# Kernel tuning notes

Hardware: AMD Instinct MI355X
Metric: run time of the kernel (lower is better)

The kernel has to match this reference:

```python
import jax, jax.numpy as jnp
import numpy as np

NUM_HEADS = 16   # matches init_kwargs
WARP_Q = 32      # per-warp Q quant granularity (rows)
BLK_K = 64       # per-block K quant granularity (rows)
EPS = 1e-8


def setup_inputs() -> dict:
    key = jax.random.key(0)
    kq, kk, kv = jax.random.split(key, 3)
    b, s, hid = 2, 2048, 2048
    q = jax.random.normal(kq, (b, s, hid), jnp.float32)
    k = jax.random.normal(kk, (b, s, hid), jnp.float32)
    v = jax.random.normal(kv, (b, s, hid), jnp.float32)
    return {"q": q, "k": k, "v": v, "window_left": 1024, "window_right": 1024}


def _quant_int8(x, group):
    # x: [b, h, s, d] -> int8-valued floats + per-row scales [b, h, s, 1]
    b, h, s, d = x.shape
    xg = x.reshape(b, h, s // group, group, d)
    scale = jnp.maximum(jnp.max(jnp.abs(xg), axis=(3, 4), keepdims=True) / 127.0, EPS)
    xq = jnp.clip(jnp.round(xg / scale), -127.0, 127.0)
    scale_rows = jnp.broadcast_to(scale, (b, h, s // group, group, 1)).reshape(b, h, s, 1)
    return xq.reshape(b, h, s, d), scale_rows


def _sage_attention(q, k, v, window_left, window_right):
    b, s, hid = q.shape
    n = NUM_HEADS
    d = hid // n
    sm_scale = 1.0 / np.sqrt(d)
    # [b, s, n*d] -> [b, n, s, d]
    qh = q.reshape(b, s, n, d).transpose(0, 2, 1, 3)
    kh = k.reshape(b, s, n, d).transpose(0, 2, 1, 3)
    vh = v.reshape(b, s, n, d).transpose(0, 2, 1, 3)

    # smooth K: subtract per-channel seq mean (softmax-invariant)
    k_mean = jnp.mean(kh, axis=2, keepdims=True)
    ks = kh - k_mean

    # per-warp int8 quantization of Q and K
    qq, q_scale = _quant_int8(qh, WARP_Q)
    kq, k_scale = _quant_int8(ks, BLK_K)

    # int8 QK^T, dequantized: [b, n, s, s]
    scores = jnp.einsum('bhid,bhjd->bhij', qq, kq)
    scores = scores * q_scale * jnp.swapaxes(k_scale, -1, -2) * sm_scale

    # sliding window mask (window < 0 means unlimited on that side)
    i = jnp.arange(s)[:, None]
    j = jnp.arange(s)[None, :]
    allowed = jnp.ones((s, s), dtype=bool)
    if window_left >= 0:
        allowed = allowed & ((i - j) <= window_left)
    if window_right >= 0:
        allowed = allowed & ((j - i) <= window_right)
    scores = jnp.where(allowed, scores, -jnp.inf)

    p = jax.nn.softmax(scores, axis=-1)

    # smooth V + fp16 PV accumulation
    v_mean = jnp.mean(vh, axis=2, keepdims=True)
    out16 = jnp.matmul(p.astype(jnp.float16), (vh - v_mean).astype(jnp.float16),
                       preferred_element_type=jnp.float16)
    out = out16.astype(jnp.float32) + v_mean  # rows of p sum to 1

    # [b, n, s, d] -> [b, s, n*d]
    return out.transpose(0, 2, 1, 3).reshape(b, s, n * d)


def reference(q, k, v, window_left, window_right):
    return _sage_attention(q, k, v, window_left, window_right)
```

## Files before the change

### kernel.cpp

```cpp
#include <hip/hip_runtime.h>
#include <hip/hip_fp16.h>
#include <math.h>

#define S_LEN 2048
#define NHID  2048
#define D_HEAD 128
#define N_BH  32
#define EPS_Q 1e-8f

typedef _Float16 half8 __attribute__((ext_vector_type(8)));
typedef _Float16 half4 __attribute__((ext_vector_type(4)));
typedef float floatx4 __attribute__((ext_vector_type(4)));

__global__ void means_kernel(const float* __restrict__ kk, const float* __restrict__ vv,
                             float* __restrict__ ksumP, float* __restrict__ vsumP) {
  int blk = blockIdx.x;
  int bh = blk >> 4, chunk = blk & 15;
  int b = bh >> 4, h = bh & 15;
  int t = threadIdx.x;
  int d4 = t & 31, sg = t >> 5;
  int s0 = chunk * 128;
  const long base = ((long)(b * S_LEN + s0)) * NHID + h * D_HEAD + d4 * 4;
  floatx4 ks = {0.f,0.f,0.f,0.f}, vs = {0.f,0.f,0.f,0.f};
  #pragma unroll 4
  for (int j = 0; j < 16; ++j) {
    long idx = base + (long)(sg * 16 + j) * NHID;
    ks += *(const floatx4*)(kk + idx);
    vs += *(const floatx4*)(vv + idx);
  }
  __shared__ floatx4 red[256];
  red[t] = ks; __syncthreads();
  if (t < 128) red[t] += red[t + 128]; __syncthreads();
  if (t < 64)  red[t] += red[t + 64];  __syncthreads();
  if (t < 32) *(floatx4*)(ksumP + (long)blk * 128 + t * 4) = red[t] + red[t + 32];
  __syncthreads();
  red[t] = vs; __syncthreads();
  if (t < 128) red[t] += red[t + 128]; __syncthreads();
  if (t < 64)  red[t] += red[t + 64];  __syncthreads();
  if (t < 32) *(floatx4*)(vsumP + (long)blk * 128 + t * 4) = red[t] + red[t + 32];
}

__global__ void prep_kernel(const float* __restrict__ q, const float* __restrict__ k,
                            const float* __restrict__ v,
                            const float* __restrict__ ksumP, const float* __restrict__ vsumP,
                            _Float16* __restrict__ qq, _Float16* __restrict__ kq,
                            _Float16* __restrict__ vt,
                            float* __restrict__ qscale, float* __restrict__ kscale,
                            float* __restrict__ vmean) {
  int blk = blockIdx.x;
  int t = threadIdx.x;
  int lane = t & 63, wid = t >> 6;
  __shared__ float wred[4];
  __shared__ __align__(16) _Float16 tile[64 * 136];
  int d4 = t & 31, sg = t >> 5;

  if (blk < 2048) {
    int bh = blk >> 6, g = blk & 63;
    int b = bh >> 4, h = bh & 15;
    int s0 = g * 32;
    const long gbase = ((long)(b * S_LEN + s0)) * NHID + h * D_HEAD + d4 * 4;
    floatx4 vals[4]; float am = 0.f;
    #pragma unroll
    for (int j = 0; j < 4; ++j) {
      floatx4 x = *(const floatx4*)(q + gbase + (long)(sg + j * 8) * NHID);
      vals[j] = x;
      am = fmaxf(am, fmaxf(fmaxf(fabsf(x[0]), fabsf(x[1])), fmaxf(fabsf(x[2]), fabsf(x[3]))));
    }
    #pragma unroll
    for (int off = 1; off < 64; off <<= 1) am = fmaxf(am, __shfl_xor(am, off, 64));
    if (lane == 0) wred[wid] = am;
    __syncthreads();
    am = fmaxf(fmaxf(wred[0], wred[1]), fmaxf(wred[2], wred[3]));
    float scale = fmaxf(am / 127.0f, EPS_Q);
    if (t == 0) qscale[bh * 64 + g] = scale;
    float inv = 1.0f / scale;
    #pragma unroll
    for (int j = 0; j < 4; ++j) {
      half4 hv;
      #pragma unroll
      for (int c = 0; c < 4; ++c)
        hv[c] = (_Float16)fminf(fmaxf(rintf(vals[j][c] * inv), -127.f), 127.f);
      *(half4*)(qq + ((long)bh * S_LEN + s0 + sg + j * 8) * D_HEAD + d4 * 4) = hv;
    }
  } else if (blk < 3072) {
    int bb = blk - 2048;
    int bh = bb >> 5, g = bb & 31;
    int b = bh >> 4, h = bh & 15;
    int s0 = g * 64;
    floatx4 msum = {0.f,0.f,0.f,0.f};
    #pragma unroll
    for (int c = 0; c < 16; ++c)
      msum += *(const floatx4*)(ksumP + (long)(bh * 16 + c) * 128 + d4 * 4);
    floatx4 mean = msum * (1.0f / 2048.0f);
    const long gbase = ((long)(b * S_LEN + s0)) * NHID + h * D_HEAD + d4 * 4;
    floatx4 vals[8]; float am = 0.f;
    #pragma unroll
    for (int j = 0; j < 8; ++j) {
      floatx4 x = *(const floatx4*)(k + gbase + (long)(sg + j * 8) * NHID) - mean;
      vals[j] = x;
      am = fmaxf(am, fmaxf(fmaxf(fabsf(x[0]), fabsf(x[1])), fmaxf(fabsf(x[2]), fabsf(x[3]))));
    }
    #pragma unroll
    for (int off = 1; off < 64; off <<= 1) am = fmaxf(am, __shfl_xor(am, off, 64));
    if (lane == 0) wred[wid] = am;
    __syncthreads();
    am = fmaxf(fmaxf(wred[0], wred[1]), fmaxf(wred[2], wred[3]));
    float scale = fmaxf(am / 127.0f, EPS_Q);
    if (t == 0) kscale[bh * 32 + g] = scale;
    float inv = 1.0f / scale;
    #pragma unroll
    for (int j = 0; j < 8; ++j) {
      half4 hv;
      #pragma unroll
      for (int c = 0; c < 4; ++c)
        hv[c] = (_Float16)fminf(fmaxf(rintf(vals[j][c] * inv), -127.f), 127.f);
      *(half4*)(kq + ((long)bh * S_LEN + s0 + sg + j * 8) * D_HEAD + d4 * 4) = hv;
    }
  } else {
    int bb = blk - 3072;
    int bh = bb >> 5, st = bb & 31;
    int b = bh >> 4, h = bh & 15;
    int s0 = st * 64;
    floatx4 msum = {0.f,0.f,0.f,0.f};
    #pragma unroll
    for (int c = 0; c < 16; ++c)
      msum += *(const floatx4*)(vsumP + (long)(bh * 16 + c) * 128 + d4 * 4);
    floatx4 mean = msum * (1.0f / 2048.0f);
    if (st == 0 && sg == 0)
      *(floatx4*)(vmean + bh * D_HEAD + d4 * 4) = mean;
    const long gbase = ((long)(b * S_LEN + s0)) * NHID + h * D_HEAD + d4 * 4;
    #pragma unroll
    for (int j = 0; j < 8; ++j) {
      floatx4 x = *(const floatx4*)(v + gbase + (long)(sg + j * 8) * NHID) - mean;
      half4 hv = { (_Float16)x[0], (_Float16)x[1], (_Float16)x[2], (_Float16)x[3] };
      *(half4*)(tile + (sg + j * 8) * 136 + d4 * 4) = hv;
    }
    __syncthreads();
    int dr = t >> 1, sh = (t & 1) * 32;
    _Float16* dst = vt + ((long)bh * D_HEAD + dr) * S_LEN + s0 + sh;
    #pragma unroll
    for (int jo = 0; jo < 4; ++jo) {
      union { half8 v8; _Float16 h[8]; } u;
      #pragma unroll
      for (int ji = 0; ji < 8; ++ji) u.h[ji] = tile[(sh + jo * 8 + ji) * 136 + dr];
      *(half8*)(dst + jo * 8) = u.v8;
    }
  }
}

__launch_bounds__(256, 2)
__global__ void attn_kernel(const _Float16* __restrict__ qq, const _Float16* __restrict__ kq,
                            const _Float16* __restrict__ vt,
                            const float* __restrict__ qscale, const float* __restrict__ kscale,
                            const float* __restrict__ vmean,
                            const int* __restrict__ wlp, const int* __restrict__ wrp,
                            float* __restrict__ out) {
  int bid = blockIdx.x;
  int xcd = bid & 7, rest = bid >> 3;
  int bh = xcd * 4 + (rest & 3);
  int qb = rest >> 2;
  int b = bh >> 4, h = bh & 15;
  int q0 = qb * 128;

  int wl = *wlp; if (wl < 0) wl = S_LEN;
  int wr = *wrp; if (wr < 0) wr = S_LEN;

  int t = threadIdx.x;
  int wv = t >> 6;
  int lane = t & 63;
  int ln = lane & 15;
  int qd = lane >> 4;

  int r0 = q0 + wv * 32;

  __shared__ __align__(16) _Float16 Kl[64 * 128];
  __shared__ __align__(16) _Float16 Vl[128 * 64];

  half8 qa[2][4];
  #pragma unroll
  for (int mh = 0; mh < 2; ++mh) {
    const _Float16* qbase = qq + ((long)bh * S_LEN + r0 + mh * 16 + ln) * D_HEAD + qd * 8;
    #pragma unroll
    for (int ks = 0; ks < 4; ++ks)
      qa[mh][ks] = *(const half8*)(qbase + ks * 32);
  }
  float qs = qscale[bh * 64 + (r0 >> 5)];

  float mrow[2];
  floatx4 lacc[2];
  floatx4 oacc[2][8];
  #pragma unroll
  for (int mh = 0; mh < 2; ++mh) {
    mrow[mh] = -1e30f;
    #pragma unroll
    for (int r = 0; r < 4; ++r) lacc[mh][r] = 0.f;
    #pragma unroll
    for (int nd = 0; nd < 8; ++nd) oacc[mh][nd] = (floatx4){0.f,0.f,0.f,0.f};
  }

  int lo = q0 - wl; if (lo < 0) lo = 0;
  int hi = q0 + 127 + wr; if (hi > S_LEN - 1) hi = S_LEN - 1;
  int t_lo = lo >> 6, t_hi = hi >> 6;

  const float sm_scale = 0.08838834764831845f;
  const _Float16* kbase = kq + (long)bh * S_LEN * D_HEAD;
  const _Float16* vbase = vt + (long)bh * D_HEAD * S_LEN;
  const float* kscb = kscale + bh * 32;
  const half8 vones = { (_Float16)1, (_Float16)1, (_Float16)1, (_Float16)1,
                        (_Float16)1, (_Float16)1, (_Float16)1, (_Float16)1 };

  half8 kpre[4], vpre[4];
  {
    int j0 = t_lo * 64;
    #pragma unroll
    for (int c = 0; c < 4; ++c) {
      int gc = t + c * 256;
      kpre[c] = *(const half8*)(kbase + (long)(j0 + (gc >> 4)) * D_HEAD + (gc & 15) * 8);
      vpre[c] = *(const half8*)(vbase + (long)(gc >> 3) * S_LEN + j0 + (gc & 7) * 8);
    }
  }

  for (int tt = t_lo; tt <= t_hi; ++tt) {
    int j0 = tt * 64;
    __syncthreads();
    #pragma unroll
    for (int c = 0; c < 4; ++c) {
      int gc = t + c * 256;
      {
        int row = gc >> 4, ci = gc & 15;
        int cs = (ci & 8) | ((ci ^ row) & 7);
        *(half8*)(Kl + row * 128 + cs * 8) = kpre[c];
      }
      {
        int row = gc >> 3, ci = gc & 7;
        int cs = (ci ^ row) & 7;
        *(half8*)(Vl + row * 64 + cs * 8) = vpre[c];
      }
    }
    __syncthreads();
    if (tt < t_hi) {
      int j1 = j0 + 64;
      #pragma unroll
      for (int c = 0; c < 4; ++c) {
        int gc = t + c * 256;
        kpre[c] = *(const half8*)(kbase + (long)(j1 + (gc >> 4)) * D_HEAD + (gc & 15) * 8);
        vpre[c] = *(const half8*)(vbase + (long)(gc >> 3) * S_LEN + j1 + (gc & 7) * 8);
      }
    }

    if (j0 + 63 < r0 - wl || j0 > r0 + 31 + wr) continue;

    float dscale = qs * kscb[tt] * sm_scale;

    floatx4 sacc[2][4];
    #pragma unroll
    for (int mh = 0; mh < 2; ++mh)
      #pragma unroll
      for (int nb = 0; nb < 4; ++nb) sacc[mh][nb] = (floatx4){0.f,0.f,0.f,0.f};
    #pragma unroll
    for (int nb = 0; nb < 4; ++nb)
      #pragma unroll
      for (int ks = 0; ks < 4; ++ks) {
        int ci = ks * 4 + qd;
        int cs = (ci & 8) | ((ci ^ ln) & 7);
        half8 kf = *(const half8*)(Kl + (nb * 16 + ln) * 128 + cs * 8);
        sacc[0][nb] = __builtin_amdgcn_mfma_f32_16x16x32_f16(kf, qa[0][ks], sacc[0][nb], 0, 0, 0);
        sacc[1][nb] = __builtin_amdgcn_mfma_f32_16x16x32_f16(kf, qa[1][ks], sacc[1][nb], 0, 0, 0);
      }

    half8 pa[2][2];
    #pragma unroll
    for (int mh = 0; mh < 2; ++mh) {
      int rb = r0 + mh * 16;
      bool need_mask = (j0 < rb + 15 - wl) || (j0 + 63 > rb + wr);
      int row = rb + ln;
      float sv[4][4];
      float mnb[4];
      #pragma unroll
      for (int nb = 0; nb < 4; ++nb) {
        #pragma unroll
        for (int r = 0; r < 4; ++r) {
          float s = sacc[mh][nb][r] * dscale;
          if (need_mask) {
            int col = j0 + nb * 16 + qd * 4 + r;
            bool ok = (row - col <= wl) && (col - row <= wr);
            s = ok ? s : -1e30f;
          }
          sv[nb][r] = s;
        }
        mnb[nb] = fmaxf(fmaxf(sv[nb][0], sv[nb][1]), fmaxf(sv[nb][2], sv[nb][3]));
      }
      float mx = fmaxf(fmaxf(mnb[0], mnb[1]), fmaxf(mnb[2], mnb[3]));
      mx = fmaxf(mx, __shfl_xor(mx, 16, 64));
      mx = fmaxf(mx, __shfl_xor(mx, 32, 64));

      if (__any(mx > mrow[mh] + 8.0f)) {
        float mnew = fmaxf(mrow[mh], mx);
        float alpha = __expf(mrow[mh] - mnew);
        mrow[mh] = mnew;
        float ar[4];
        #pragma unroll
        for (int r = 0; r < 4; ++r) ar[r] = __shfl(alpha, qd * 4 + r, 64);
        #pragma unroll
        for (int nd = 0; nd < 8; ++nd) {
          floatx4 o = oacc[mh][nd];
          #pragma unroll
          for (int r = 0; r < 4; ++r) o[r] *= ar[r];
          oacc[mh][nd] = o;
        }
        #pragma unroll
        for (int r = 0; r < 4; ++r) lacc[mh][r] *= ar[r];
      }

      float m0 = mrow[mh];
      #pragma unroll
      for (int ks = 0; ks < 2; ++ks) {
        half8 tf;
        #pragma unroll
        for (int r = 0; r < 4; ++r) {
          tf[r]     = (_Float16)__expf(sv[2 * ks][r] - m0);
          tf[4 + r] = (_Float16)__expf(sv[2 * ks + 1][r] - m0);
        }
        pa[mh][ks] = tf;
      }
    }

    #pragma unroll
    for (int nd = 0; nd < 8; ++nd) {
      int rowv = nd * 16 + ln;
      #pragma unroll
      for (int ks = 0; ks < 2; ++ks) {
        int ci0 = ks * 4 + (qd >> 1);
        int o4 = (qd & 1) * 4;
        int cs0 = (ci0 ^ rowv) & 7;
        int cs1 = ((ci0 + 2) ^ rowv) & 7;
        half4 v0 = *(const half4*)(Vl + rowv * 64 + cs0 * 8 + o4);
        half4 v1 = *(const half4*)(Vl + rowv * 64 + cs1 * 8 + o4);
        half8 vf = { v0[0], v0[1], v0[2], v0[3], v1[0], v1[1], v1[2], v1[3] };
        oacc[0][nd] = __builtin_amdgcn_mfma_f32_16x16x32_f16(pa[0][ks], vf, oacc[0][nd], 0, 0, 0);
        oacc[1][nd] = __builtin_amdgcn_mfma_f32_16x16x32_f16(pa[1][ks], vf, oacc[1][nd], 0, 0, 0);
      }
    }
    #pragma unroll
    for (int mh = 0; mh < 2; ++mh) {
      lacc[mh] = __builtin_amdgcn_mfma_f32_16x16x32_f16(pa[mh][0], vones, lacc[mh], 0, 0, 0);
      lacc[mh] = __builtin_amdgcn_mfma_f32_16x16x32_f16(pa[mh][1], vones, lacc[mh], 0, 0, 0);
    }
  }

  float vm[8];
  #pragma unroll
  for (int nd = 0; nd < 8; ++nd)
    vm[nd] = vmean[bh * D_HEAD + nd * 16 + ln];
  float* obase = out + ((long)b * S_LEN) * NHID + h * D_HEAD;
  #pragma unroll
  for (int mh = 0; mh < 2; ++mh)
    #pragma unroll
    for (int r = 0; r < 4; ++r) {
      int row = r0 + mh * 16 + qd * 4 + r;
      float linv = 1.0f / lacc[mh][r];
      #pragma unroll
      for (int nd = 0; nd < 8; ++nd) {
        float o16 = (float)(_Float16)(oacc[mh][nd][r] * linv);
        obase[(long)row * NHID + nd * 16 + ln] = o16 + vm[nd];
      }
    }
}

extern "C" void kernel_launch(void* const* d_in, const int* in_sizes, int n_in,
                              void* d_out, int out_size, void* d_ws, size_t ws_size,
                              hipStream_t stream) {
  (void)in_sizes; (void)n_in; (void)out_size; (void)ws_size;
  const float* q = (const float*)d_in[0];
  const float* k = (const float*)d_in[1];
  const float* v = (const float*)d_in[2];
  const int* wl = (const int*)d_in[3];
  const int* wr = (const int*)d_in[4];
  float* out = (float*)d_out;

  char* ws = (char*)d_ws;
  size_t off = 0;
  const size_t tensz = (size_t)N_BH * S_LEN * D_HEAD * sizeof(_Float16);
  _Float16* qq = (_Float16*)(ws + off); off += tensz;
  _Float16* kq = (_Float16*)(ws + off); off += tensz;
  _Float16* vt = (_Float16*)(ws + off); off += tensz;
  float* ksumP  = (float*)(ws + off); off += (size_t)N_BH * 16 * 128 * sizeof(float);
  float* vsumP  = (float*)(ws + off); off += (size_t)N_BH * 16 * 128 * sizeof(float);
  float* vmean  = (float*)(ws + off); off += N_BH * D_HEAD * sizeof(float);
  float* qscale = (float*)(ws + off); off += N_BH * 64 * sizeof(float);
  float* kscale = (float*)(ws + off); off += N_BH * 32 * sizeof(float);

  means_kernel<<<512, 256, 0, stream>>>(k, v, ksumP, vsumP);
  prep_kernel<<<4096, 256, 0, stream>>>(q, k, v, ksumP, vsumP, qq, kq, vt, qscale, kscale, vmean);
  attn_kernel<<<512, 256, 0, stream>>>(qq, kq, vt, qscale, kscale, vmean, wl, wr, out);
}
```

Measured before the change: 246.4 us.

## Split KV range across two half-blocks and merge softmax partials in shared memory

Doubles the attention block to 512 threads. Each half of the block processes half of the key tiles for the same 128 query rows, and the two partial results are merged through shared memory with a max/rescale combine (a split-K flash-decoding style). The aim is more waves in flight per CU and a shorter serial loop per block, since 512 blocks is only about two per CU. The cost is 64KB of LDS plus extra syncs and an epilogue merge, and launch_bounds(512,4) may force register spilling given the large accumulator arrays.

```diff
diff --git a/kernel.cpp b/kernel.cpp
--- a/kernel.cpp
+++ b/kernel.cpp
@@ -148,7 +148,7 @@
   }
 }
 
-__launch_bounds__(256, 2)
+__launch_bounds__(512, 4)
 __global__ void attn_kernel(const _Float16* __restrict__ qq, const _Float16* __restrict__ kq,
                             const _Float16* __restrict__ vt,
                             const float* __restrict__ qscale, const float* __restrict__ kscale,
@@ -167,14 +167,21 @@
 
   int t = threadIdx.x;
   int wv = t >> 6;
+  int hf = wv >> 2;
+  int wv4 = wv & 3;
+  int th = t & 255;
   int lane = t & 63;
   int ln = lane & 15;
   int qd = lane >> 4;
 
-  int r0 = q0 + wv * 32;
-
-  __shared__ __align__(16) _Float16 Kl[64 * 128];
-  __shared__ __align__(16) _Float16 Vl[128 * 64];
+  int r0 = q0 + wv4 * 32;
+
+  __shared__ __align__(16) char smem[65536];
+  __shared__ float Mhi[4][32];
+  __shared__ float Mmax[4][32];
+  __shared__ float Lhi[4][32];
+  _Float16* KlH = (_Float16*)(smem + hf * 32768);
+  _Float16* VlH = (_Float16*)(smem + hf * 32768 + 16384);
 
   half8 qa[2][4];
   #pragma unroll
@@ -201,6 +208,10 @@
   int lo = q0 - wl; if (lo < 0) lo = 0;
   int hi = q0 + 127 + wr; if (hi > S_LEN - 1) hi = S_LEN - 1;
   int t_lo = lo >> 6, t_hi = hi >> 6;
+  int n = t_hi - t_lo + 1;
+  int nh = (n + 1) >> 1;
+  int sh0 = t_lo + hf * nh;
+  int cl = hf ? (n - nh) : nh;
 
   const float sm_scale = 0.08838834764831845f;
   const _Float16* kbase = kq + (long)bh * S_LEN * D_HEAD;
@@ -211,42 +222,47 @@
 
   half8 kpre[4], vpre[4];
   {
-    int j0 = t_lo * 64;
+    int tp = sh0 > t_hi ? t_hi : sh0;
+    int j0 = tp * 64;
     #pragma unroll
     for (int c = 0; c < 4; ++c) {
-      int gc = t + c * 256;
+      int gc = th + c * 256;
       kpre[c] = *(const half8*)(kbase + (long)(j0 + (gc >> 4)) * D_HEAD + (gc & 15) * 8);
       vpre[c] = *(const half8*)(vbase + (long)(gc >> 3) * S_LEN + j0 + (gc & 7) * 8);
     }
   }
 
-  for (int tt = t_lo; tt <= t_hi; ++tt) {
+  for (int i = 0; i < nh; ++i) {
+    int tt = sh0 + i;
     int j0 = tt * 64;
     __syncthreads();
-    #pragma unroll
-    for (int c = 0; c < 4; ++c) {
-      int gc = t + c * 256;
-      {
-        int row = gc >> 4, ci = gc & 15;
-        int cs = (ci & 8) | ((ci ^ row) & 7);
-        *(half8*)(Kl + row * 128 + cs * 8) = kpre[c];
-      }
-      {
-        int row = gc >> 3, ci = gc & 7;
-        int cs = (ci ^ row) & 7;
-        *(half8*)(Vl + row * 64 + cs * 8) = vpre[c];
+    if (i < cl) {
+      #pragma unroll
+      for (int c = 0; c < 4; ++c) {
+        int gc = th + c * 256;
+        {
+          int row = gc >> 4, ci = gc & 15;
+          int cs = (ci & 8) | ((ci ^ row) & 7);
+          *(half8*)(KlH + row * 128 + cs * 8) = kpre[c];
+        }
+        {
+          int row = gc >> 3, ci = gc & 7;
+          int cs = (ci ^ row) & 7;
+          *(half8*)(VlH + row * 64 + cs * 8) = vpre[c];
+        }
       }
     }
     __syncthreads();
-    if (tt < t_hi) {
+    if (i + 1 < cl) {
       int j1 = j0 + 64;
       #pragma unroll
       for (int c = 0; c < 4; ++c) {
-        int gc = t + c * 256;
+        int gc = th + c * 256;
         kpre[c] = *(const half8*)(kbase + (long)(j1 + (gc >> 4)) * D_HEAD + (gc & 15) * 8);
         vpre[c] = *(const half8*)(vbase + (long)(gc >> 3) * S_LEN + j1 + (gc & 7) * 8);
       }
     }
+    if (i >= cl) continue;
 
     if (j0 + 63 < r0 - wl || j0 > r0 + 31 + wr) continue;
 
@@ -263,7 +279,7 @@
       for (int ks = 0; ks < 4; ++ks) {
         int ci = ks * 4 + qd;
         int cs = (ci & 8) | ((ci ^ ln) & 7);
-        half8 kf = *(const half8*)(Kl + (nb * 16 + ln) * 128 + cs * 8);
+        half8 kf = *(const half8*)(KlH + (nb * 16 + ln) * 128 + cs * 8);
         sacc[0][nb] = __builtin_amdgcn_mfma_f32_16x16x32_f16(kf, qa[0][ks], sacc[0][nb], 0, 0, 0);
         sacc[1][nb] = __builtin_amdgcn_mfma_f32_16x16x32_f16(kf, qa[1][ks], sacc[1][nb], 0, 0, 0);
       }
@@ -334,8 +350,8 @@
         int o4 = (qd & 1) * 4;
         int cs0 = (ci0 ^ rowv) & 7;
         int cs1 = ((ci0 + 2) ^ rowv) & 7;
-        half4 v0 = *(const half4*)(Vl + rowv * 64 + cs0 * 8 + o4);
-        half4 v1 = *(const half4*)(Vl + rowv * 64 + cs1 * 8 + o4);
+        half4 v0 = *(const half4*)(VlH + rowv * 64 + cs0 * 8 + o4);
+        half4 v1 = *(const half4*)(VlH + rowv * 64 + cs1 * 8 + o4);
         half8 vf = { v0[0], v0[1], v0[2], v0[3], v1[0], v1[1], v1[2], v1[3] };
         oacc[0][nd] = __builtin_amdgcn_mfma_f32_16x16x32_f16(pa[0][ks], vf, oacc[0][nd], 0, 0, 0);
         oacc[1][nd] = __builtin_amdgcn_mfma_f32_16x16x32_f16(pa[1][ks], vf, oacc[1][nd], 0, 0, 0);
@@ -348,23 +364,78 @@
     }
   }
 
-  float vm[8];
+  float* Ocmb = (float*)smem;
+  __syncthreads();
+  if (hf == 1 && qd == 0) {
+    Mhi[wv4][ln] = mrow[0];
+    Mhi[wv4][16 + ln] = mrow[1];
+  }
+  __syncthreads();
+  float mmax[2];
+  if (hf == 0) {
+    #pragma unroll
+    for (int mh = 0; mh < 2; ++mh)
+      mmax[mh] = fmaxf(mrow[mh], Mhi[wv4][mh * 16 + ln]);
+    if (qd == 0) {
+      Mmax[wv4][ln] = mmax[0];
+      Mmax[wv4][16 + ln] = mmax[1];
+    }
+  }
+  __syncthreads();
+  if (hf == 1) {
+    #pragma unroll
+    for (int mh = 0; mh < 2; ++mh) mmax[mh] = Mmax[wv4][mh * 16 + ln];
+  }
+  float ar[2][4];
   #pragma unroll
-  for (int nd = 0; nd < 8; ++nd)
-    vm[nd] = vmean[bh * D_HEAD + nd * 16 + ln];
-  float* obase = out + ((long)b * S_LEN) * NHID + h * D_HEAD;
-  #pragma unroll
-  for (int mh = 0; mh < 2; ++mh)
-    #pragma unroll
-    for (int r = 0; r < 4; ++r) {
-      int row = r0 + mh * 16 + qd * 4 + r;
-      float linv = 1.0f / lacc[mh][r];
-      #pragma unroll
-      for (int nd = 0; nd < 8; ++nd) {
-        float o16 = (float)(_Float16)(oacc[mh][nd][r] * linv);
-        obase[(long)row * NHID + nd * 16 + ln] = o16 + vm[nd];
-      }
-    }
+  for (int mh = 0; mh < 2; ++mh) {
+    float al = __expf(mrow[mh] - mmax[mh]);
+    #pragma unroll
+    for (int r = 0; r < 4; ++r) ar[mh][r] = __shfl(al, qd * 4 + r, 64);
+  }
+  if (hf == 1) {
+    #pragma unroll
+    for (int mh = 0; mh < 2; ++mh) {
+      #pragma unroll
+      for (int nd = 0; nd < 8; ++nd)
+        #pragma unroll
+        for (int r = 0; r < 4; ++r) {
+          int rw = mh * 16 + qd * 4 + r;
+          int col = nd * 16 + ln;
+          int csw = (col + rw * 4) & 127;
+          Ocmb[(wv4 * 32 + rw) * 128 + csw] = oacc[mh][nd][r] * ar[mh][r];
+        }
+      if (ln == 0)
+        #pragma unroll
+        for (int r = 0; r < 4; ++r)
+          Lhi[wv4][mh * 16 + qd * 4 + r] = lacc[mh][r] * ar[mh][r];
+    }
+  }
+  __syncthreads();
+  if (hf == 0) {
+    float vm[8];
+    #pragma unroll
+    for (int nd = 0; nd < 8; ++nd)
+      vm[nd] = vmean[bh * D_HEAD + nd * 16 + ln];
+    float* obase = out + ((long)b * S_LEN) * NHID + h * D_HEAD;
+    #pragma unroll
+    for (int mh = 0; mh < 2; ++mh)
+      #pragma unroll
+      for (int r = 0; r < 4; ++r) {
+        int rw = mh * 16 + qd * 4 + r;
+        float lsum = lacc[mh][r] * ar[mh][r] + Lhi[wv4][rw];
+        float linv = 1.0f / lsum;
+        int row = r0 + rw;
+        #pragma unroll
+        for (int nd = 0; nd < 8; ++nd) {
+          int col = nd * 16 + ln;
+          int csw = (col + rw * 4) & 127;
+          float o = oacc[mh][nd][r] * ar[mh][r] + Ocmb[(wv4 * 32 + rw) * 128 + csw];
+          float o16 = (float)(_Float16)(o * linv);
+          obase[(long)row * NHID + col] = o16 + vm[nd];
+        }
+      }
+  }
 }
 
 extern "C" void kernel_launch(void* const* d_in, const int* in_sizes, int n_in,
@@ -392,5 +463,5 @@
 
   means_kernel<<<512, 256, 0, stream>>>(k, v, ksumP, vsumP);
   prep_kernel<<<4096, 256, 0, stream>>>(q, k, v, ksumP, vsumP, qq, kq, vt, qscale, kscale, vmean);
-  attn_kernel<<<512, 256, 0, stream>>>(qq, kq, vt, qscale, kscale, vmean, wl, wr, out);
+  attn_kernel<<<512, 512, 0, stream>>>(qq, kq, vt, qscale, kscale, vmean, wl, wr, out);
 }
```

Result: slower. 635.7 us (+158.1%).

## Double-buffer K/V shared tiles, fold log2e into scale, add MFMA priority hints

Applied to the files above, without the earlier changes.

Doubles the shared-memory K and V tiles so the next tile is staged into the alternate buffer while the current one is computed, which drops one of the two barriers per iteration. The softmax scale now includes log2(e) so the exponentials can use the native exp2 instruction. s_setprio hints raise wave priority around the MFMA sections. The cost is twice the LDS (64 KB per block), which may lower occupancy, plus longer register live ranges from holding prefetched data across the compute.

```diff
diff --git a/kernel.cpp b/kernel.cpp
--- a/kernel.cpp
+++ b/kernel.cpp
@@ -173,8 +173,8 @@
 
   int r0 = q0 + wv * 32;
 
-  __shared__ __align__(16) _Float16 Kl[64 * 128];
-  __shared__ __align__(16) _Float16 Vl[128 * 64];
+  __shared__ __align__(16) _Float16 Kl[2][64 * 128];
+  __shared__ __align__(16) _Float16 Vl[2][128 * 64];
 
   half8 qa[2][4];
   #pragma unroll
@@ -202,7 +202,7 @@
   int hi = q0 + 127 + wr; if (hi > S_LEN - 1) hi = S_LEN - 1;
   int t_lo = lo >> 6, t_hi = hi >> 6;
 
-  const float sm_scale = 0.08838834764831845f;
+  const float sm_scale2 = 0.08838834764831845f * 1.4426950408889634f;
   const _Float16* kbase = kq + (long)bh * S_LEN * D_HEAD;
   const _Float16* vbase = vt + (long)bh * D_HEAD * S_LEN;
   const float* kscb = kscale + bh * 32;
@@ -210,142 +210,154 @@
                         (_Float16)1, (_Float16)1, (_Float16)1, (_Float16)1 };
 
   half8 kpre[4], vpre[4];
-  {
-    int j0 = t_lo * 64;
-    #pragma unroll
-    for (int c = 0; c < 4; ++c) {
-      int gc = t + c * 256;
-      kpre[c] = *(const half8*)(kbase + (long)(j0 + (gc >> 4)) * D_HEAD + (gc & 15) * 8);
-      vpre[c] = *(const half8*)(vbase + (long)(gc >> 3) * S_LEN + j0 + (gc & 7) * 8);
-    }
-  }
+
+#define LOAD_PRE(TILE)                                                              \
+  {                                                                                 \
+    int j0_ = (TILE) * 64;                                                          \
+    _Pragma("unroll")                                                               \
+    for (int c = 0; c < 4; ++c) {                                                   \
+      int gc = t + c * 256;                                                         \
+      kpre[c] = *(const half8*)(kbase + (long)(j0_ + (gc >> 4)) * D_HEAD + (gc & 15) * 8); \
+      vpre[c] = *(const half8*)(vbase + (long)(gc >> 3) * S_LEN + j0_ + (gc & 7) * 8);     \
+    }                                                                               \
+  }
+
+#define STAGE_TO(BB)                                                                \
+  {                                                                                 \
+    _Float16* Kb = &Kl[BB][0];                                                      \
+    _Float16* Vb = &Vl[BB][0];                                                      \
+    _Pragma("unroll")                                                               \
+    for (int c = 0; c < 4; ++c) {                                                   \
+      int gc = t + c * 256;                                                         \
+      { int row = gc >> 4, ci = gc & 15;                                            \
+        int cs = (ci & 8) | ((ci ^ row) & 7);                                       \
+        *(half8*)(Kb + row * 128 + cs * 8) = kpre[c]; }                             \
+      { int row = gc >> 3, ci = gc & 7;                                             \
+        int cs = (ci ^ row) & 7;                                                    \
+        *(half8*)(Vb + row * 64 + cs * 8) = vpre[c]; }                              \
+    }                                                                               \
+  }
+
+  LOAD_PRE(t_lo);
+  STAGE_TO(0);
+  __syncthreads();
+  if (t_lo + 1 <= t_hi) LOAD_PRE(t_lo + 1);
 
   for (int tt = t_lo; tt <= t_hi; ++tt) {
     int j0 = tt * 64;
+    int cur = (tt - t_lo) & 1;
+
+    if (tt + 1 <= t_hi) {
+      STAGE_TO(cur ^ 1);
+      if (tt + 2 <= t_hi) LOAD_PRE(tt + 2);
+    }
+
+    if (!(j0 + 63 < r0 - wl || j0 > r0 + 31 + wr)) {
+      const _Float16* Kc = &Kl[cur][0];
+      const _Float16* Vc = &Vl[cur][0];
+      float dscale2 = qs * kscb[tt] * sm_scale2;
+
+      floatx4 sacc[2][4];
+      #pragma unroll
+      for (int mh = 0; mh < 2; ++mh)
+        #pragma unroll
+        for (int nb = 0; nb < 4; ++nb) sacc[mh][nb] = (floatx4){0.f,0.f,0.f,0.f};
+      __builtin_amdgcn_s_setprio(1);
+      #pragma unroll
+      for (int nb = 0; nb < 4; ++nb)
+        #pragma unroll
+        for (int ks = 0; ks < 4; ++ks) {
+          int ci = ks * 4 + qd;
+          int cs = (ci & 8) | ((ci ^ ln) & 7);
+          half8 kf = *(const half8*)(Kc + (nb * 16 + ln) * 128 + cs * 8);
+          sacc[0][nb] = __builtin_amdgcn_mfma_f32_16x16x32_f16(kf, qa[0][ks], sacc[0][nb], 0, 0, 0);
+          sacc[1][nb] = __builtin_amdgcn_mfma_f32_16x16x32_f16(kf, qa[1][ks], sacc[1][nb], 0, 0, 0);
+        }
+      __builtin_amdgcn_s_setprio(0);
+
+      half8 pa[2][2];
+      #pragma unroll
+      for (int mh = 0; mh < 2; ++mh) {
+        int rb = r0 + mh * 16;
+        bool need_mask = (j0 < rb + 15 - wl) || (j0 + 63 > rb + wr);
+        int row = rb + ln;
+        float sv[4][4];
+        float mnb[4];
+        #pragma unroll
+        for (int nb = 0; nb < 4; ++nb) {
+          #pragma unroll
+          for (int r = 0; r < 4; ++r) {
+            float s = sacc[mh][nb][r] * dscale2;
+            if (need_mask) {
+              int col = j0 + nb * 16 + qd * 4 + r;
+              bool ok = (row - col <= wl) && (col - row <= wr);
+              s = ok ? s : -1e30f;
+            }
+            sv[nb][r] = s;
+          }
+          mnb[nb] = fmaxf(fmaxf(sv[nb][0], sv[nb][1]), fmaxf(sv[nb][2], sv[nb][3]));
+        }
+        float mx = fmaxf(fmaxf(mnb[0], mnb[1]), fmaxf(mnb[2], mnb[3]));
+        mx = fmaxf(mx, __shfl_xor(mx, 16, 64));
+        mx = fmaxf(mx, __shfl_xor(mx, 32, 64));
+
+        if (__any(mx > mrow[mh] + 8.0f)) {
+          float mnew = fmaxf(mrow[mh], mx);
+          float alpha = __builtin_amdgcn_exp2f(mrow[mh] - mnew);
+          mrow[mh] = mnew;
+          float ar[4];
+          #pragma unroll
+          for (int r = 0; r < 4; ++r) ar[r] = __shfl(alpha, qd * 4 + r, 64);
+          #pragma unroll
+          for (int nd = 0; nd < 8; ++nd) {
+            floatx4 o = oacc[mh][nd];
+            #pragma unroll
+            for (int r = 0; r < 4; ++r) o[r] *= ar[r];
+            oacc[mh][nd] = o;
+          }
+          #pragma unroll
+          for (int r = 0; r < 4; ++r) lacc[mh][r] *= ar[r];
+        }
+
+        float m0 = mrow[mh];
+        #pragma unroll
+        for (int ks = 0; ks < 2; ++ks) {
+          half8 tf;
+          #pragma unroll
+          for (int r = 0; r < 4; ++r) {
+            tf[r]     = (_Float16)__builtin_amdgcn_exp2f(sv[2 * ks][r] - m0);
+            tf[4 + r] = (_Float16)__builtin_amdgcn_exp2f(sv[2 * ks + 1][r] - m0);
+          }
+          pa[mh][ks] = tf;
+        }
+      }
+
+      __builtin_amdgcn_s_setprio(1);
+      #pragma unroll
+      for (int nd = 0; nd < 8; ++nd) {
+        int rowv = nd * 16 + ln;
+        #pragma unroll
+        for (int ks = 0; ks < 2; ++ks) {
+          int ci0 = ks * 4 + (qd >> 1);
+          int o4 = (qd & 1) * 4;
+          int cs0 = (ci0 ^ rowv) & 7;
+          int cs1 = ((ci0 + 2) ^ rowv) & 7;
+          half4 v0 = *(const half4*)(Vc + rowv * 64 + cs0 * 8 + o4);
+          half4 v1 = *(const half4*)(Vc + rowv * 64 + cs1 * 8 + o4);
+          half8 vf = { v0[0], v0[1], v0[2], v0[3], v1[0], v1[1], v1[2], v1[3] };
+          oacc[0][nd] = __builtin_amdgcn_mfma_f32_16x16x32_f16(pa[0][ks], vf, oacc[0][nd], 0, 0, 0);
+          oacc[1][nd] = __builtin_amdgcn_mfma_f32_16x16x32_f16(pa[1][ks], vf, oacc[1][nd], 0, 0, 0);
+        }
+      }
+      #pragma unroll
+      for (int mh = 0; mh < 2; ++mh) {
+        lacc[mh] = __builtin_amdgcn_mfma_f32_16x16x32_f16(pa[mh][0], vones, lacc[mh], 0, 0, 0);
+        lacc[mh] = __builtin_amdgcn_mfma_f32_16x16x32_f16(pa[mh][1], vones, lacc[mh], 0, 0, 0);
+      }
+      __builtin_amdgcn_s_setprio(0);
+    }
+
     __syncthreads();
-    #pragma unroll
-    for (int c = 0; c < 4; ++c) {
-      int gc = t + c * 256;
-      {
-        int row = gc >> 4, ci = gc & 15;
-        int cs = (ci & 8) | ((ci ^ row) & 7);
-        *(half8*)(Kl + row * 128 + cs * 8) = kpre[c];
-      }
-      {
-        int row = gc >> 3, ci = gc & 7;
-        int cs = (ci ^ row) & 7;
-        *(half8*)(Vl + row * 64 + cs * 8) = vpre[c];
-      }
-    }
-    __syncthreads();
-    if (tt < t_hi) {
-      int j1 = j0 + 64;
-      #pragma unroll
-      for (int c = 0; c < 4; ++c) {
-        int gc = t + c * 256;
-        kpre[c] = *(const half8*)(kbase + (long)(j1 + (gc >> 4)) * D_HEAD + (gc & 15) * 8);
-        vpre[c] = *(const half8*)(vbase + (long)(gc >> 3) * S_LEN + j1 + (gc & 7) * 8);
-      }
-    }
-
-    if (j0 + 63 < r0 - wl || j0 > r0 + 31 + wr) continue;
-
-    float dscale = qs * kscb[tt] * sm_scale;
-
-    floatx4 sacc[2][4];
-    #pragma unroll
-    for (int mh = 0; mh < 2; ++mh)
-      #pragma unroll
-      for (int nb = 0; nb < 4; ++nb) sacc[mh][nb] = (floatx4){0.f,0.f,0.f,0.f};
-    #pragma unroll
-    for (int nb = 0; nb < 4; ++nb)
-      #pragma unroll
-      for (int ks = 0; ks < 4; ++ks) {
-        int ci = ks * 4 + qd;
-        int cs = (ci & 8) | ((ci ^ ln) & 7);
-        half8 kf = *(const half8*)(Kl + (nb * 16 + ln) * 128 + cs * 8);
-        sacc[0][nb] = __builtin_amdgcn_mfma_f32_16x16x32_f16(kf, qa[0][ks], sacc[0][nb], 0, 0, 0);
-        sacc[1][nb] = __builtin_amdgcn_mfma_f32_16x16x32_f16(kf, qa[1][ks], sacc[1][nb], 0, 0, 0);
-      }
-
-    half8 pa[2][2];
-    #pragma unroll
-    for (int mh = 0; mh < 2; ++mh) {
-      int rb = r0 + mh * 16;
-      bool need_mask = (j0 < rb + 15 - wl) || (j0 + 63 > rb + wr);
-      int row = rb + ln;
-      float sv[4][4];
-      float mnb[4];
-      #pragma unroll
-      for (int nb = 0; nb < 4; ++nb) {
-        #pragma unroll
-        for (int r = 0; r < 4; ++r) {
-          float s = sacc[mh][nb][r] * dscale;
-          if (need_mask) {
-            int col = j0 + nb * 16 + qd * 4 + r;
-            bool ok = (row - col <= wl) && (col - row <= wr);
-            s = ok ? s : -1e30f;
-          }
-          sv[nb][r] = s;
-        }
-        mnb[nb] = fmaxf(fmaxf(sv[nb][0], sv[nb][1]), fmaxf(sv[nb][2], sv[nb][3]));
-      }
-      float mx = fmaxf(fmaxf(mnb[0], mnb[1]), fmaxf(mnb[2], mnb[3]));
-      mx = fmaxf(mx, __shfl_xor(mx, 16, 64));
-      mx = fmaxf(mx, __shfl_xor(mx, 32, 64));
-
-      if (__any(mx > mrow[mh] + 8.0f)) {
-        float mnew = fmaxf(mrow[mh], mx);
-        float alpha = __expf(mrow[mh] - mnew);
-        mrow[mh] = mnew;
-        float ar[4];
-        #pragma unroll
-        for (int r = 0; r < 4; ++r) ar[r] = __shfl(alpha, qd * 4 + r, 64);
-        #pragma unroll
-        for (int nd = 0; nd < 8; ++nd) {
-          floatx4 o = oacc[mh][nd];
-          #pragma unroll
-          for (int r = 0; r < 4; ++r) o[r] *= ar[r];
-          oacc[mh][nd] = o;
-        }
-        #pragma unroll
-        for (int r = 0; r < 4; ++r) lacc[mh][r] *= ar[r];
-      }
-
-      float m0 = mrow[mh];
-      #pragma unroll
-      for (int ks = 0; ks < 2; ++ks) {
-        half8 tf;
-        #pragma unroll
-        for (int r = 0; r < 4; ++r) {
-          tf[r]     = (_Float16)__expf(sv[2 * ks][r] - m0);
-          tf[4 + r] = (_Float16)__expf(sv[2 * ks + 1][r] - m0);
-        }
-        pa[mh][ks] = tf;
-      }
-    }
-
-    #pragma unroll
-    for (int nd = 0; nd < 8; ++nd) {
-      int rowv = nd * 16 + ln;
-      #pragma unroll
-      for (int ks = 0; ks < 2; ++ks) {
-        int ci0 = ks * 4 + (qd >> 1);
-        int o4 = (qd & 1) * 4;
-        int cs0 = (ci0 ^ rowv) & 7;
-        int cs1 = ((ci0 + 2) ^ rowv) & 7;
-        half4 v0 = *(const half4*)(Vl + rowv * 64 + cs0 * 8 + o4);
-        half4 v1 = *(const half4*)(Vl + rowv * 64 + cs1 * 8 + o4);
-        half8 vf = { v0[0], v0[1], v0[2], v0[3], v1[0], v1[1], v1[2], v1[3] };
-        oacc[0][nd] = __builtin_amdgcn_mfma_f32_16x16x32_f16(pa[0][ks], vf, oacc[0][nd], 0, 0, 0);
-        oacc[1][nd] = __builtin_amdgcn_mfma_f32_16x16x32_f16(pa[1][ks], vf, oacc[1][nd], 0, 0, 0);
-      }
-    }
-    #pragma unroll
-    for (int mh = 0; mh < 2; ++mh) {
-      lacc[mh] = __builtin_amdgcn_mfma_f32_16x16x32_f16(pa[mh][0], vones, lacc[mh], 0, 0, 0);
-      lacc[mh] = __builtin_amdgcn_mfma_f32_16x16x32_f16(pa[mh][1], vones, lacc[mh], 0, 0, 0);
-    }
   }
 
   float vm[8];
@@ -365,6 +377,8 @@
         obase[(long)row * NHID + nd * 16 + ln] = o16 + vm[nd];
       }
     }
+#undef LOAD_PRE
+#undef STAGE_TO
 }
 
 extern "C" void kernel_launch(void* const* d_in, const int* in_sizes, int n_in,
```

New measurement: 249.2 us. About the same (+1.1%).

## Store Q/K as packed int8 and use int8 MFMA for QK^T

Applied to the files above, without the earlier changes.

Quantized Q and K are now stored as int8 bytes instead of fp16-valued halves. The QK^T product uses the i32 16x16x64 int8 MFMA with integer accumulators, which are converted to float before scaling. K staging in shared memory and the prefetch registers shrink by half, and the swizzle is changed to match. This halves Q/K workspace traffic and MFMA count for the score matmul. Results should stay exact because the values are integers in [-127,127].

```diff
diff --git a/kernel.cpp b/kernel.cpp
--- a/kernel.cpp
+++ b/kernel.cpp
@@ -11,6 +11,8 @@
 typedef _Float16 half8 __attribute__((ext_vector_type(8)));
 typedef _Float16 half4 __attribute__((ext_vector_type(4)));
 typedef float floatx4 __attribute__((ext_vector_type(4)));
+typedef int int4v __attribute__((ext_vector_type(4)));
+typedef signed char int8_t_;
 
 __global__ void means_kernel(const float* __restrict__ kk, const float* __restrict__ vv,
                              float* __restrict__ ksumP, float* __restrict__ vsumP) {
@@ -43,7 +45,7 @@
 __global__ void prep_kernel(const float* __restrict__ q, const float* __restrict__ k,
                             const float* __restrict__ v,
                             const float* __restrict__ ksumP, const float* __restrict__ vsumP,
-                            _Float16* __restrict__ qq, _Float16* __restrict__ kq,
+                            signed char* __restrict__ qq, signed char* __restrict__ kq,
                             _Float16* __restrict__ vt,
                             float* __restrict__ qscale, float* __restrict__ kscale,
                             float* __restrict__ vmean) {
@@ -76,11 +78,13 @@
     float inv = 1.0f / scale;
     #pragma unroll
     for (int j = 0; j < 4; ++j) {
-      half4 hv;
-      #pragma unroll
-      for (int c = 0; c < 4; ++c)
-        hv[c] = (_Float16)fminf(fmaxf(rintf(vals[j][c] * inv), -127.f), 127.f);
-      *(half4*)(qq + ((long)bh * S_LEN + s0 + sg + j * 8) * D_HEAD + d4 * 4) = hv;
+      int pk = 0;
+      #pragma unroll
+      for (int c = 0; c < 4; ++c) {
+        int qv = (int)fminf(fmaxf(rintf(vals[j][c] * inv), -127.f), 127.f);
+        pk |= (qv & 255) << (8 * c);
+      }
+      ((int*)qq)[((long)bh * S_LEN + s0 + sg + j * 8) * 32 + d4] = pk;
     }
   } else if (blk < 3072) {
     int bb = blk - 2048;
@@ -110,11 +114,13 @@
     float inv = 1.0f / scale;
     #pragma unroll
     for (int j = 0; j < 8; ++j) {
-      half4 hv;
-      #pragma unroll
-      for (int c = 0; c < 4; ++c)
-        hv[c] = (_Float16)fminf(fmaxf(rintf(vals[j][c] * inv), -127.f), 127.f);
-      *(half4*)(kq + ((long)bh * S_LEN + s0 + sg + j * 8) * D_HEAD + d4 * 4) = hv;
+      int pk = 0;
+      #pragma unroll
+      for (int c = 0; c < 4; ++c) {
+        int qv = (int)fminf(fmaxf(rintf(vals[j][c] * inv), -127.f), 127.f);
+        pk |= (qv & 255) << (8 * c);
+      }
+      ((int*)kq)[((long)bh * S_LEN + s0 + sg + j * 8) * 32 + d4] = pk;
     }
   } else {
     int bb = blk - 3072;
@@ -149,7 +155,7 @@
 }
 
 __launch_bounds__(256, 2)
-__global__ void attn_kernel(const _Float16* __restrict__ qq, const _Float16* __restrict__ kq,
+__global__ void attn_kernel(const signed char* __restrict__ qq, const signed char* __restrict__ kq,
                             const _Float16* __restrict__ vt,
                             const float* __restrict__ qscale, const float* __restrict__ kscale,
                             const float* __restrict__ vmean,
@@ -173,16 +179,16 @@
 
   int r0 = q0 + wv * 32;
 
-  __shared__ __align__(16) _Float16 Kl[64 * 128];
+  __shared__ __align__(16) signed char Kl[64 * 128];
   __shared__ __align__(16) _Float16 Vl[128 * 64];
 
-  half8 qa[2][4];
+  int4v qa8[2][2];
   #pragma unroll
   for (int mh = 0; mh < 2; ++mh) {
-    const _Float16* qbase = qq + ((long)bh * S_LEN + r0 + mh * 16 + ln) * D_HEAD + qd * 8;
-    #pragma unroll
-    for (int ks = 0; ks < 4; ++ks)
-      qa[mh][ks] = *(const half8*)(qbase + ks * 32);
+    const signed char* qbase = qq + ((long)bh * S_LEN + r0 + mh * 16 + ln) * 128 + qd * 16;
+    #pragma unroll
+    for (int ks2 = 0; ks2 < 2; ++ks2)
+      qa8[mh][ks2] = *(const int4v*)(qbase + ks2 * 64);
   }
   float qs = qscale[bh * 64 + (r0 >> 5)];
 
@@ -203,19 +209,24 @@
   int t_lo = lo >> 6, t_hi = hi >> 6;
 
   const float sm_scale = 0.08838834764831845f;
-  const _Float16* kbase = kq + (long)bh * S_LEN * D_HEAD;
+  const signed char* kbase = kq + (long)bh * S_LEN * 128;
   const _Float16* vbase = vt + (long)bh * D_HEAD * S_LEN;
   const float* kscb = kscale + bh * 32;
   const half8 vones = { (_Float16)1, (_Float16)1, (_Float16)1, (_Float16)1,
                         (_Float16)1, (_Float16)1, (_Float16)1, (_Float16)1 };
 
-  half8 kpre[4], vpre[4];
+  int4v kpre[2];
+  half8 vpre[4];
   {
     int j0 = t_lo * 64;
     #pragma unroll
+    for (int c = 0; c < 2; ++c) {
+      int gc = t + c * 256;
+      kpre[c] = *(const int4v*)(kbase + (long)(j0 + (gc >> 3)) * 128 + (gc & 7) * 16);
+    }
+    #pragma unroll
     for (int c = 0; c < 4; ++c) {
       int gc = t + c * 256;
-      kpre[c] = *(const half8*)(kbase + (long)(j0 + (gc >> 4)) * D_HEAD + (gc & 15) * 8);
       vpre[c] = *(const half8*)(vbase + (long)(gc >> 3) * S_LEN + j0 + (gc & 7) * 8);
     }
   }
@@ -224,26 +235,30 @@
     int j0 = tt * 64;
     __syncthreads();
     #pragma unroll
+    for (int c = 0; c < 2; ++c) {
+      int gc = t + c * 256;
+      int row = gc >> 3, ci = gc & 7;
+      int cs = (ci ^ row) & 7;
+      *(int4v*)(Kl + row * 128 + cs * 16) = kpre[c];
+    }
+    #pragma unroll
     for (int c = 0; c < 4; ++c) {
       int gc = t + c * 256;
-      {
-        int row = gc >> 4, ci = gc & 15;
-        int cs = (ci & 8) | ((ci ^ row) & 7);
-        *(half8*)(Kl + row * 128 + cs * 8) = kpre[c];
-      }
-      {
-        int row = gc >> 3, ci = gc & 7;
-        int cs = (ci ^ row) & 7;
-        *(half8*)(Vl + row * 64 + cs * 8) = vpre[c];
-      }
+      int row = gc >> 3, ci = gc & 7;
+      int cs = (ci ^ row) & 7;
+      *(half8*)(Vl + row * 64 + cs * 8) = vpre[c];
     }
     __syncthreads();
     if (tt < t_hi) {
       int j1 = j0 + 64;
       #pragma unroll
+      for (int c = 0; c < 2; ++c) {
+        int gc = t + c * 256;
+        kpre[c] = *(const int4v*)(kbase + (long)(j1 + (gc >> 3)) * 128 + (gc & 7) * 16);
+      }
+      #pragma unroll
       for (int c = 0; c < 4; ++c) {
         int gc = t + c * 256;
-        kpre[c] = *(const half8*)(kbase + (long)(j1 + (gc >> 4)) * D_HEAD + (gc & 15) * 8);
         vpre[c] = *(const half8*)(vbase + (long)(gc >> 3) * S_LEN + j1 + (gc & 7) * 8);
       }
     }
@@ -252,20 +267,20 @@
 
     float dscale = qs * kscb[tt] * sm_scale;
 
-    floatx4 sacc[2][4];
+    int4v isacc[2][4];
     #pragma unroll
     for (int mh = 0; mh < 2; ++mh)
       #pragma unroll
-      for (int nb = 0; nb < 4; ++nb) sacc[mh][nb] = (floatx4){0.f,0.f,0.f,0.f};
+      for (int nb = 0; nb < 4; ++nb) isacc[mh][nb] = (int4v){0,0,0,0};
     #pragma unroll
     for (int nb = 0; nb < 4; ++nb)
       #pragma unroll
-      for (int ks = 0; ks < 4; ++ks) {
-        int ci = ks * 4 + qd;
-        int cs = (ci & 8) | ((ci ^ ln) & 7);
-        half8 kf = *(const half8*)(Kl + (nb * 16 + ln) * 128 + cs * 8);
-        sacc[0][nb] = __builtin_amdgcn_mfma_f32_16x16x32_f16(kf, qa[0][ks], sacc[0][nb], 0, 0, 0);
-        sacc[1][nb] = __builtin_amdgcn_mfma_f32_16x16x32_f16(kf, qa[1][ks], sacc[1][nb], 0, 0, 0);
+      for (int ks2 = 0; ks2 < 2; ++ks2) {
+        int ci = ks2 * 4 + qd;
+        int cs = (ci ^ ln) & 7;
+        int4v kf = *(const int4v*)(Kl + (nb * 16 + ln) * 128 + cs * 16);
+        isacc[0][nb] = __builtin_amdgcn_mfma_i32_16x16x64_i8(kf, qa8[0][ks2], isacc[0][nb], 0, 0, 0);
+        isacc[1][nb] = __builtin_amdgcn_mfma_i32_16x16x64_i8(kf, qa8[1][ks2], isacc[1][nb], 0, 0, 0);
       }
 
     half8 pa[2][2];
@@ -280,7 +295,7 @@
       for (int nb = 0; nb < 4; ++nb) {
         #pragma unroll
         for (int r = 0; r < 4; ++r) {
-          float s = sacc[mh][nb][r] * dscale;
+          float s = (float)isacc[mh][nb][r] * dscale;
           if (need_mask) {
             int col = j0 + nb * 16 + qd * 4 + r;
             bool ok = (row - col <= wl) && (col - row <= wr);
@@ -380,10 +395,11 @@
 
   char* ws = (char*)d_ws;
   size_t off = 0;
-  const size_t tensz = (size_t)N_BH * S_LEN * D_HEAD * sizeof(_Float16);
-  _Float16* qq = (_Float16*)(ws + off); off += tensz;
-  _Float16* kq = (_Float16*)(ws + off); off += tensz;
-  _Float16* vt = (_Float16*)(ws + off); off += tensz;
+  const size_t i8sz = (size_t)N_BH * S_LEN * D_HEAD;
+  const size_t f16sz = (size_t)N_BH * S_LEN * D_HEAD * sizeof(_Float16);
+  signed char* qq = (signed char*)(ws + off); off += i8sz;
+  signed char* kq = (signed char*)(ws + off); off += i8sz;
+  _Float16* vt = (_Float16*)(ws + off); off += f16sz;
   float* ksumP  = (float*)(ws + off); off += (size_t)N_BH * 16 * 128 * sizeof(float);
   float* vsumP  = (float*)(ws + off); off += (size_t)N_BH * 16 * 128 * sizeof(float);
   float* vmean  = (float*)(ws + off); off += N_BH * D_HEAD * sizeof(float);
```

After: 237.0 us. 1.04x faster.
